# Kernel optimization log

Hardware: AMD Instinct MI355X
Metric: run time of the kernel (lower is better)

## Reference

```python
import jax, jax.numpy as jnp
import numpy as np

GROUPS = 32
EPS = 1e-5


def setup_inputs() -> dict:
    key = jax.random.key(0)
    k1, k2, k3, k4, k5 = jax.random.split(key, 5)
    B, C, H, W = 16, 256, 80, 80
    cg = C // GROUPS  # 8 channels per group
    x = jax.random.normal(k1, (B, C, H, W), dtype=jnp.float32)
    # conv1x1: Conv2d(cg, cg, 1) -> weight [cg, cg], bias [cg]
    fan_in = cg
    bound = 1.0 / np.sqrt(fan_in)
    conv_w = jax.random.uniform(k2, (cg, cg), minval=-bound, maxval=bound, dtype=jnp.float32)
    conv_b = jax.random.uniform(k3, (cg,), minval=-bound, maxval=bound, dtype=jnp.float32)
    # GroupNorm(num_groups=cg, num_channels=cg) affine params (init: ones/zeros)
    gn_w = jnp.ones((cg,), dtype=jnp.float32)
    gn_b = jnp.zeros((cg,), dtype=jnp.float32)
    return {"x": x, "conv_w": conv_w, "conv_b": conv_b, "gn_w": gn_w, "gn_b": gn_b}


def reference(x, conv_w, conv_b, gn_w, gn_b):
    b, c, h, w = x.shape
    cg = c // GROUPS
    gx = x.reshape(b * GROUPS, cg, h, w)  # [bg, cg, h, w]

    def norm(t):
        # GroupNorm with num_groups == num_channels: per-channel norm over (h, w)
        mu = jnp.mean(t, axis=(2, 3), keepdims=True)
        var = jnp.var(t, axis=(2, 3), keepdims=True)
        tn = (t - mu) * jax.lax.rsqrt(var + EPS)
        return tn * gn_w[None, :, None, None] + gn_b[None, :, None, None]

    def gate_branch(ph, pw):
        # ph: [bg, cg, h] (pooled over w), pw: [bg, cg, w] (pooled over h)
        cat = jnp.concatenate([ph, pw], axis=2)  # [bg, cg, h+w]
        hw = jnp.einsum('bcl,oc->bol', cat, conv_w) + conv_b[None, :, None]
        gh, gw = hw[:, :, :h], hw[:, :, h:]
        gated = gx * jax.nn.sigmoid(gh)[..., None] * jax.nn.sigmoid(gw)[:, :, None, :]
        return norm(gated)

    # avg-pool branch
    x1 = gate_branch(jnp.mean(gx, axis=3), jnp.mean(gx, axis=2))
    # max-pool branch
    y1 = gate_branch(jnp.max(gx, axis=3), jnp.max(gx, axis=2))

    x11 = x1.reshape(b * GROUPS, cg, h * w)
    y11 = y1.reshape(b * GROUPS, cg, h * w)
    # channel-attention vectors: softmax over the cg channel axis
    x12 = jax.nn.softmax(jnp.mean(x1, axis=(2, 3)), axis=-1)  # [bg, cg]  (avg pool)
    y12 = jax.nn.softmax(jnp.max(y1, axis=(2, 3)), axis=-1)   # [bg, cg]  (max pool)

    weights = jnp.einsum('bc,bcl->bl', x12, y11) + jnp.einsum('bc,bcl->bl', y12, x11)
    weights = weights.reshape(b * GROUPS, 1, h, w)
    return (gx * jax.nn.sigmoid(weights)).reshape(b, c, h, w)
```

## Files before the change

kernel.cpp:

```cpp
#include <hip/hip_runtime.h>
#include <math.h>

constexpr int CG   = 8;
constexpr int Hh   = 80;
constexpr int HW   = 6400;
constexpr int NG   = 512;
constexpr int NCH  = NG * CG;
constexpr int PP   = NCH * 80;
constexpr float EPSf = 1e-5f;

constexpr int COEF = 4 * PP;

__device__ __forceinline__ float sigmoidf(float v) {
    return 1.0f / (1.0f + __expf(-v));
}

__global__ __launch_bounds__(256) void k_pool(const float* __restrict__ x,
                                              float* __restrict__ ws) {
    const int bgc = blockIdx.x;
    const float* base = x + (size_t)bgc * HW;
    __shared__ float tile[Hh * 84];

    for (int v = threadIdx.x; v < 1600; v += 256) {
        int h  = v / 20;
        int w0 = (v % 20) * 4;
        float4 d = ((const float4*)base)[v];
        *(float4*)&tile[h * 84 + w0] = d;
    }
    __syncthreads();

    const int t = threadIdx.x;
    if (t < 80) {
        float s = 0.f, m = -INFINITY;
        const float4* r = (const float4*)&tile[t * 84];
        #pragma unroll
        for (int i = 0; i < 20; i++) {
            float4 d = r[i];
            s += d.x + d.y + d.z + d.w;
            m = fmaxf(m, fmaxf(fmaxf(d.x, d.y), fmaxf(d.z, d.w)));
        }
        ws[0 * PP + bgc * 80 + t] = s * (1.f / 80.f);
        ws[2 * PP + bgc * 80 + t] = m;
    } else if (t >= 128 && t < 208) {
        const int c = t - 128;
        float s2 = 0.f, m2 = -INFINITY;
        #pragma unroll 8
        for (int i = 0; i < 80; i++) {
            float v = tile[i * 84 + c];
            s2 += v;
            m2 = fmaxf(m2, v);
        }
        ws[1 * PP + bgc * 80 + c] = s2 * (1.f / 80.f);
        ws[3 * PP + bgc * 80 + c] = m2;
    }
}

__global__ __launch_bounds__(512) void k_mid(const float* __restrict__ x,
                                             const float* __restrict__ conv_w,
                                             const float* __restrict__ conv_b,
                                             const float* __restrict__ gnw,
                                             const float* __restrict__ gnb,
                                             float* __restrict__ ws) {
    const int bg  = blockIdx.x;
    const int tid = threadIdx.x;

    __shared__ float pl[4 * 640];
    __shared__ float g[4 * 640];
    __shared__ float wsm[64];
    __shared__ float cbs[8];
    __shared__ float stats[8][6];
    __shared__ float Axs[8], Bxs[8], Ays[8], Bys[8], ymaxs[8], cHx[8], cHy[8];
    __shared__ float kcs;

    if (tid < 64) wsm[tid] = conv_w[tid];
    if (tid < 8)  cbs[tid] = conv_b[tid];

    #pragma unroll
    for (int i = 0; i < 5; ++i) {
        const int e = tid + i * 512;
        if (e < 2560) {
            const int a = e / 640, rem = e % 640, c = rem / 80, p = rem % 80;
            pl[e] = ws[a * PP + (bg * 8 + c) * 80 + p];
        }
    }
    __syncthreads();

    #pragma unroll
    for (int i = 0; i < 5; ++i) {
        const int e = tid + i * 512;
        if (e < 2560) {
            const int rem = e % 640, a = e / 640, c = rem / 80, p = rem % 80;
            float acc = cbs[c];
            #pragma unroll
            for (int cc = 0; cc < 8; ++cc)
                acc += wsm[c * 8 + cc] * pl[a * 640 + cc * 80 + p];
            g[e] = sigmoidf(acc);
        }
    }
    __syncthreads();

    {
        const int c = tid >> 6, lane = tid & 63;
        const float* cb_ = x + (size_t)(bg * 8 + c) * HW;
        float s1x = 0.f, s2x = 0.f, s1y = 0.f, s2y = 0.f;
        float my = -INFINITY, ny = INFINITY;
        for (int j = 0; j < 25; ++j) {
            const int v = lane + j * 64;
            float4 d = ((const float4*)cb_)[v];
            const int h = v / 20, w0 = (v % 20) * 4;
            const float ghx = g[0 * 640 + c * 80 + h];
            const float ghy = g[2 * 640 + c * 80 + h];
            const float4 gwx = *(const float4*)&g[1 * 640 + c * 80 + w0];
            const float4 gwy = *(const float4*)&g[3 * 640 + c * 80 + w0];
            const float dd[4]  = {d.x, d.y, d.z, d.w};
            const float gx4[4] = {gwx.x, gwx.y, gwx.z, gwx.w};
            const float gy4[4] = {gwy.x, gwy.y, gwy.z, gwy.w};
            #pragma unroll
            for (int k = 0; k < 4; ++k) {
                const float tx = dd[k] * ghx * gx4[k];
                const float ty = dd[k] * ghy * gy4[k];
                s1x += tx; s2x += tx * tx;
                s1y += ty; s2y += ty * ty;
                my = fmaxf(my, ty); ny = fminf(ny, ty);
            }
        }
        #pragma unroll
        for (int off = 32; off > 0; off >>= 1) {
            s1x += __shfl_down(s1x, off);
            s2x += __shfl_down(s2x, off);
            s1y += __shfl_down(s1y, off);
            s2y += __shfl_down(s2y, off);
            my = fmaxf(my, __shfl_down(my, off));
            ny = fminf(ny, __shfl_down(ny, off));
        }
        if (lane == 0) {
            stats[c][0] = s1x; stats[c][1] = s2x; stats[c][2] = s1y;
            stats[c][3] = s2y; stats[c][4] = my;  stats[c][5] = ny;
        }
    }
    __syncthreads();

    if (tid < 8) {
        const float s1x = stats[tid][0], s2x = stats[tid][1];
        const float s1y = stats[tid][2], s2y = stats[tid][3];
        const float my  = stats[tid][4], ny  = stats[tid][5];
        const float w = gnw[tid], b = gnb[tid];
        const float mux  = s1x * (1.f / 6400.f);
        const float varx = s2x * (1.f / 6400.f) - mux * mux;
        const float ax   = rsqrtf(varx + EPSf) * w;
        Axs[tid] = ax; Bxs[tid] = b - mux * ax;
        const float muy  = s1y * (1.f / 6400.f);
        const float vary = s2y * (1.f / 6400.f) - muy * muy;
        const float ay   = rsqrtf(vary + EPSf) * w;
        Ays[tid] = ay; Bys[tid] = b - muy * ay;
        ymaxs[tid] = (ay >= 0.f ? my : ny) * ay + Bys[tid];
    }
    __syncthreads();
    if (tid == 0) {
        float x12[8], y12[8];
        float mb = -INFINITY;
        for (int c = 0; c < 8; ++c) mb = fmaxf(mb, gnb[c]);
        float se = 0.f;
        for (int c = 0; c < 8; ++c) { x12[c] = __expf(gnb[c] - mb); se += x12[c]; }
        float inv = 1.f / se;
        for (int c = 0; c < 8; ++c) x12[c] *= inv;
        float m2 = -INFINITY;
        for (int c = 0; c < 8; ++c) m2 = fmaxf(m2, ymaxs[c]);
        se = 0.f;
        for (int c = 0; c < 8; ++c) { y12[c] = __expf(ymaxs[c] - m2); se += y12[c]; }
        inv = 1.f / se;
        float kc = 0.f;
        for (int c = 0; c < 8; ++c) {
            y12[c] *= inv;
            cHx[c] = y12[c] * Axs[c];
            cHy[c] = x12[c] * Ays[c];
            kc += x12[c] * Bys[c] + y12[c] * Bxs[c];
        }
        kcs = kc;
    }
    __syncthreads();
    for (int e = tid; e < 640; e += 512) {
        g[e]        *= cHx[e / 80];
        g[1280 + e] *= cHy[e / 80];
    }
    __syncthreads();

    float* cf = ws + COEF + (size_t)bg * 2568;
    #pragma unroll
    for (int i = 0; i < 5; ++i) {
        const int e = tid + i * 512;
        if (e < 2560) cf[e] = g[e];
    }
    if (tid == 0) cf[2560] = kcs;
}

__global__ __launch_bounds__(256) void k_out(const float* __restrict__ x,
                                             const float* __restrict__ ws,
                                             float* __restrict__ out) {
    const int bg = blockIdx.x >> 2;
    const int q  = blockIdx.x & 3;
    const int tid = threadIdx.x;

    __shared__ float g[2560];
    __shared__ float kcs;
    const float* cf = ws + COEF + (size_t)bg * 2568;
    #pragma unroll
    for (int i = 0; i < 10; ++i) {
        const int e = tid + i * 256;
        if (e < 2560) g[e] = cf[e];
    }
    if (tid == 0) kcs = cf[2560];
    __syncthreads();

    const float kc = kcs;
    const float* base = x + (size_t)bg * CG * HW;
    float*       ob   = out + (size_t)bg * CG * HW;

    #pragma unroll
    for (int i = 0; i < 2; ++i) {
        const int v = q * 400 + tid + i * 256;
        if (v < (q + 1) * 400) {
            const int h = v / 20, w0 = (v % 20) * 4;
            float4 gxv[8];
            #pragma unroll
            for (int c = 0; c < 8; ++c)
                gxv[c] = *(const float4*)(base + c * HW + v * 4);

            float s0 = kc, s1 = kc, s2 = kc, s3 = kc;
            #pragma unroll
            for (int c = 0; c < 8; ++c) {
                const float chx = g[0 * 640 + c * 80 + h];
                const float chy = g[2 * 640 + c * 80 + h];
                const float4 cwx = *(const float4*)&g[1 * 640 + c * 80 + w0];
                const float4 cwy = *(const float4*)&g[3 * 640 + c * 80 + w0];
                s0 += gxv[c].x * (chy * cwy.x + chx * cwx.x);
                s1 += gxv[c].y * (chy * cwy.y + chx * cwx.y);
                s2 += gxv[c].z * (chy * cwy.z + chx * cwx.z);
                s3 += gxv[c].w * (chy * cwy.w + chx * cwx.w);
            }
            s0 = sigmoidf(s0); s1 = sigmoidf(s1);
            s2 = sigmoidf(s2); s3 = sigmoidf(s3);
            #pragma unroll
            for (int c = 0; c < 8; ++c) {
                float4 o;
                o.x = gxv[c].x * s0; o.y = gxv[c].y * s1;
                o.z = gxv[c].z * s2; o.w = gxv[c].w * s3;
                *(float4*)(ob + c * HW + v * 4) = o;
            }
        }
    }
}

extern "C" void kernel_launch(void* const* d_in, const int* in_sizes, int n_in,
                              void* d_out, int out_size, void* d_ws, size_t ws_size,
                              hipStream_t stream) {
    const float* x      = (const float*)d_in[0];
    const float* conv_w = (const float*)d_in[1];
    const float* conv_b = (const float*)d_in[2];
    const float* gn_w   = (const float*)d_in[3];
    const float* gn_b   = (const float*)d_in[4];
    float* out = (float*)d_out;
    float* ws  = (float*)d_ws;

    k_pool<<<NCH,    256, 0, stream>>>(x, ws);
    k_mid <<<NG,     512, 0, stream>>>(x, conv_w, conv_b, gn_w, gn_b, ws);
    k_out <<<NG * 4, 256, 0, stream>>>(x, ws, out);
}
```

Measured before the change: 79.27 us.

## Fuse mid and output kernels, keeping the group's x tile in registers

Merges k_mid and k_out into a single 1024-thread kernel per group. Each thread loads its slice of x (8 channels by up to 2 float4 positions) into registers once and reuses it for the gated-statistics pass and the final output pass. This removes a second full read of x and the round trip of the coefficients through the workspace. In exchange it uses only 512 blocks with heavy register pressure (64 floats of x per thread plus 1024-thread blocks), and the statistics reduction now goes across 16 waves per channel.

```diff
diff --git a/kernel.cpp b/kernel.cpp
--- a/kernel.cpp
+++ b/kernel.cpp
@@ -8,8 +8,6 @@
 constexpr int NCH  = NG * CG;
 constexpr int PP   = NCH * 80;
 constexpr float EPSf = 1e-5f;
-
-constexpr int COEF = 4 * PP;
 
 __device__ __forceinline__ float sigmoidf(float v) {
     return 1.0f / (1.0f + __expf(-v));
@@ -55,41 +53,53 @@
     }
 }
 
-__global__ __launch_bounds__(512) void k_mid(const float* __restrict__ x,
-                                             const float* __restrict__ conv_w,
-                                             const float* __restrict__ conv_b,
-                                             const float* __restrict__ gnw,
-                                             const float* __restrict__ gnb,
-                                             float* __restrict__ ws) {
+__global__ __launch_bounds__(1024, 4) void k_rest(
+    const float* __restrict__ x,
+    const float* __restrict__ conv_w,
+    const float* __restrict__ conv_b,
+    const float* __restrict__ gnw,
+    const float* __restrict__ gnb,
+    const float* __restrict__ ws,
+    float* __restrict__ out)
+{
     const int bg  = blockIdx.x;
     const int tid = threadIdx.x;
 
-    __shared__ float pl[4 * 640];
-    __shared__ float g[4 * 640];
+    __shared__ float pl[2560];
+    __shared__ float g[2560];
     __shared__ float wsm[64];
     __shared__ float cbs[8];
-    __shared__ float stats[8][6];
+    __shared__ float red[16][8][6];
     __shared__ float Axs[8], Bxs[8], Ays[8], Bys[8], ymaxs[8], cHx[8], cHy[8];
     __shared__ float kcs;
 
     if (tid < 64) wsm[tid] = conv_w[tid];
     if (tid < 8)  cbs[tid] = conv_b[tid];
-
-    #pragma unroll
-    for (int i = 0; i < 5; ++i) {
-        const int e = tid + i * 512;
+    #pragma unroll
+    for (int i = 0; i < 3; ++i) {
+        const int e = tid + i * 1024;
         if (e < 2560) {
             const int a = e / 640, rem = e % 640, c = rem / 80, p = rem % 80;
             pl[e] = ws[a * PP + (bg * 8 + c) * 80 + p];
         }
     }
-    __syncthreads();
-
-    #pragma unroll
-    for (int i = 0; i < 5; ++i) {
-        const int e = tid + i * 512;
+
+    const float* base = x + (size_t)bg * CG * HW;
+    const int s0 = tid, s1 = tid + 1024;
+    float4 xr0[8], xr1[8];
+    #pragma unroll
+    for (int c = 0; c < 8; ++c) xr0[c] = ((const float4*)(base + c * HW))[s0];
+    if (tid < 576) {
+        #pragma unroll
+        for (int c = 0; c < 8; ++c) xr1[c] = ((const float4*)(base + c * HW))[s1];
+    }
+    __syncthreads();
+
+    #pragma unroll
+    for (int i = 0; i < 3; ++i) {
+        const int e = tid + i * 1024;
         if (e < 2560) {
-            const int rem = e % 640, a = e / 640, c = rem / 80, p = rem % 80;
+            const int a = e / 640, rem = e % 640, c = rem / 80, p = rem % 80;
             float acc = cbs[c];
             #pragma unroll
             for (int cc = 0; cc < 8; ++cc)
@@ -99,20 +109,18 @@
     }
     __syncthreads();
 
-    {
-        const int c = tid >> 6, lane = tid & 63;
-        const float* cb_ = x + (size_t)(bg * 8 + c) * HW;
+    const int h0 = s0 / 20, w00 = (s0 % 20) * 4;
+    const int h1 = s1 / 20, w01 = (s1 % 20) * 4;
+    const int wv = tid >> 6, lane = tid & 63;
+    #pragma unroll
+    for (int c = 0; c < 8; ++c) {
         float s1x = 0.f, s2x = 0.f, s1y = 0.f, s2y = 0.f;
         float my = -INFINITY, ny = INFINITY;
-        for (int j = 0; j < 25; ++j) {
-            const int v = lane + j * 64;
-            float4 d = ((const float4*)cb_)[v];
-            const int h = v / 20, w0 = (v % 20) * 4;
-            const float ghx = g[0 * 640 + c * 80 + h];
-            const float ghy = g[2 * 640 + c * 80 + h];
-            const float4 gwx = *(const float4*)&g[1 * 640 + c * 80 + w0];
-            const float4 gwy = *(const float4*)&g[3 * 640 + c * 80 + w0];
-            const float dd[4]  = {d.x, d.y, d.z, d.w};
+        {
+            const float ghx = g[c * 80 + h0],  ghy = g[1280 + c * 80 + h0];
+            const float4 gwx = *(const float4*)&g[640  + c * 80 + w00];
+            const float4 gwy = *(const float4*)&g[1920 + c * 80 + w00];
+            const float dd[4]  = {xr0[c].x, xr0[c].y, xr0[c].z, xr0[c].w};
             const float gx4[4] = {gwx.x, gwx.y, gwx.z, gwx.w};
             const float gy4[4] = {gwy.x, gwy.y, gwy.z, gwy.w};
             #pragma unroll
@@ -124,6 +132,22 @@
                 my = fmaxf(my, ty); ny = fminf(ny, ty);
             }
         }
+        if (tid < 576) {
+            const float ghx = g[c * 80 + h1],  ghy = g[1280 + c * 80 + h1];
+            const float4 gwx = *(const float4*)&g[640  + c * 80 + w01];
+            const float4 gwy = *(const float4*)&g[1920 + c * 80 + w01];
+            const float dd[4]  = {xr1[c].x, xr1[c].y, xr1[c].z, xr1[c].w};
+            const float gx4[4] = {gwx.x, gwx.y, gwx.z, gwx.w};
+            const float gy4[4] = {gwy.x, gwy.y, gwy.z, gwy.w};
+            #pragma unroll
+            for (int k = 0; k < 4; ++k) {
+                const float tx = dd[k] * ghx * gx4[k];
+                const float ty = dd[k] * ghy * gy4[k];
+                s1x += tx; s2x += tx * tx;
+                s1y += ty; s2y += ty * ty;
+                my = fmaxf(my, ty); ny = fminf(ny, ty);
+            }
+        }
         #pragma unroll
         for (int off = 32; off > 0; off >>= 1) {
             s1x += __shfl_down(s1x, off);
@@ -134,26 +158,32 @@
             ny = fminf(ny, __shfl_down(ny, off));
         }
         if (lane == 0) {
-            stats[c][0] = s1x; stats[c][1] = s2x; stats[c][2] = s1y;
-            stats[c][3] = s2y; stats[c][4] = my;  stats[c][5] = ny;
+            red[wv][c][0] = s1x; red[wv][c][1] = s2x; red[wv][c][2] = s1y;
+            red[wv][c][3] = s2y; red[wv][c][4] = my;  red[wv][c][5] = ny;
         }
     }
     __syncthreads();
 
     if (tid < 8) {
-        const float s1x = stats[tid][0], s2x = stats[tid][1];
-        const float s1y = stats[tid][2], s2y = stats[tid][3];
-        const float my  = stats[tid][4], ny  = stats[tid][5];
+        float a0 = 0.f, a1 = 0.f, a2 = 0.f, a3 = 0.f;
+        float a4 = -INFINITY, a5 = INFINITY;
+        #pragma unroll
+        for (int w2 = 0; w2 < 16; ++w2) {
+            a0 += red[w2][tid][0]; a1 += red[w2][tid][1];
+            a2 += red[w2][tid][2]; a3 += red[w2][tid][3];
+            a4 = fmaxf(a4, red[w2][tid][4]);
+            a5 = fminf(a5, red[w2][tid][5]);
+        }
         const float w = gnw[tid], b = gnb[tid];
-        const float mux  = s1x * (1.f / 6400.f);
-        const float varx = s2x * (1.f / 6400.f) - mux * mux;
+        const float mux  = a0 * (1.f / 6400.f);
+        const float varx = a1 * (1.f / 6400.f) - mux * mux;
         const float ax   = rsqrtf(varx + EPSf) * w;
         Axs[tid] = ax; Bxs[tid] = b - mux * ax;
-        const float muy  = s1y * (1.f / 6400.f);
-        const float vary = s2y * (1.f / 6400.f) - muy * muy;
+        const float muy  = a2 * (1.f / 6400.f);
+        const float vary = a3 * (1.f / 6400.f) - muy * muy;
         const float ay   = rsqrtf(vary + EPSf) * w;
         Ays[tid] = ay; Bys[tid] = b - muy * ay;
-        ymaxs[tid] = (ay >= 0.f ? my : ny) * ay + Bys[tid];
+        ymaxs[tid] = (ay >= 0.f ? a4 : a5) * ay + Bys[tid];
     }
     __syncthreads();
     if (tid == 0) {
@@ -179,74 +209,56 @@
         kcs = kc;
     }
     __syncthreads();
-    for (int e = tid; e < 640; e += 512) {
-        g[e]        *= cHx[e / 80];
-        g[1280 + e] *= cHy[e / 80];
-    }
-    __syncthreads();
-
-    float* cf = ws + COEF + (size_t)bg * 2568;
-    #pragma unroll
-    for (int i = 0; i < 5; ++i) {
-        const int e = tid + i * 512;
-        if (e < 2560) cf[e] = g[e];
-    }
-    if (tid == 0) cf[2560] = kcs;
-}
-
-__global__ __launch_bounds__(256) void k_out(const float* __restrict__ x,
-                                             const float* __restrict__ ws,
-                                             float* __restrict__ out) {
-    const int bg = blockIdx.x >> 2;
-    const int q  = blockIdx.x & 3;
-    const int tid = threadIdx.x;
-
-    __shared__ float g[2560];
-    __shared__ float kcs;
-    const float* cf = ws + COEF + (size_t)bg * 2568;
-    #pragma unroll
-    for (int i = 0; i < 10; ++i) {
-        const int e = tid + i * 256;
-        if (e < 2560) g[e] = cf[e];
-    }
-    if (tid == 0) kcs = cf[2560];
+    if (tid < 640) {
+        g[tid]        *= cHx[tid / 80];
+        g[1280 + tid] *= cHy[tid / 80];
+    }
     __syncthreads();
 
     const float kc = kcs;
-    const float* base = x + (size_t)bg * CG * HW;
-    float*       ob   = out + (size_t)bg * CG * HW;
-
-    #pragma unroll
-    for (int i = 0; i < 2; ++i) {
-        const int v = q * 400 + tid + i * 256;
-        if (v < (q + 1) * 400) {
-            const int h = v / 20, w0 = (v % 20) * 4;
-            float4 gxv[8];
-            #pragma unroll
-            for (int c = 0; c < 8; ++c)
-                gxv[c] = *(const float4*)(base + c * HW + v * 4);
-
-            float s0 = kc, s1 = kc, s2 = kc, s3 = kc;
-            #pragma unroll
-            for (int c = 0; c < 8; ++c) {
-                const float chx = g[0 * 640 + c * 80 + h];
-                const float chy = g[2 * 640 + c * 80 + h];
-                const float4 cwx = *(const float4*)&g[1 * 640 + c * 80 + w0];
-                const float4 cwy = *(const float4*)&g[3 * 640 + c * 80 + w0];
-                s0 += gxv[c].x * (chy * cwy.x + chx * cwx.x);
-                s1 += gxv[c].y * (chy * cwy.y + chx * cwx.y);
-                s2 += gxv[c].z * (chy * cwy.z + chx * cwx.z);
-                s3 += gxv[c].w * (chy * cwy.w + chx * cwx.w);
-            }
-            s0 = sigmoidf(s0); s1 = sigmoidf(s1);
-            s2 = sigmoidf(s2); s3 = sigmoidf(s3);
-            #pragma unroll
-            for (int c = 0; c < 8; ++c) {
-                float4 o;
-                o.x = gxv[c].x * s0; o.y = gxv[c].y * s1;
-                o.z = gxv[c].z * s2; o.w = gxv[c].w * s3;
-                *(float4*)(ob + c * HW + v * 4) = o;
-            }
+    float* ob = out + (size_t)bg * CG * HW;
+    {
+        float u0 = kc, u1 = kc, u2 = kc, u3 = kc;
+        #pragma unroll
+        for (int c = 0; c < 8; ++c) {
+            const float chx = g[c * 80 + h0], chy = g[1280 + c * 80 + h0];
+            const float4 cwx = *(const float4*)&g[640  + c * 80 + w00];
+            const float4 cwy = *(const float4*)&g[1920 + c * 80 + w00];
+            u0 += xr0[c].x * (chy * cwy.x + chx * cwx.x);
+            u1 += xr0[c].y * (chy * cwy.y + chx * cwx.y);
+            u2 += xr0[c].z * (chy * cwy.z + chx * cwx.z);
+            u3 += xr0[c].w * (chy * cwy.w + chx * cwx.w);
+        }
+        u0 = sigmoidf(u0); u1 = sigmoidf(u1);
+        u2 = sigmoidf(u2); u3 = sigmoidf(u3);
+        #pragma unroll
+        for (int c = 0; c < 8; ++c) {
+            float4 o;
+            o.x = xr0[c].x * u0; o.y = xr0[c].y * u1;
+            o.z = xr0[c].z * u2; o.w = xr0[c].w * u3;
+            ((float4*)(ob + c * HW))[s0] = o;
+        }
+    }
+    if (tid < 576) {
+        float u0 = kc, u1 = kc, u2 = kc, u3 = kc;
+        #pragma unroll
+        for (int c = 0; c < 8; ++c) {
+            const float chx = g[c * 80 + h1], chy = g[1280 + c * 80 + h1];
+            const float4 cwx = *(const float4*)&g[640  + c * 80 + w01];
+            const float4 cwy = *(const float4*)&g[1920 + c * 80 + w01];
+            u0 += xr1[c].x * (chy * cwy.x + chx * cwx.x);
+            u1 += xr1[c].y * (chy * cwy.y + chx * cwx.y);
+            u2 += xr1[c].z * (chy * cwy.z + chx * cwx.z);
+            u3 += xr1[c].w * (chy * cwy.w + chx * cwx.w);
+        }
+        u0 = sigmoidf(u0); u1 = sigmoidf(u1);
+        u2 = sigmoidf(u2); u3 = sigmoidf(u3);
+        #pragma unroll
+        for (int c = 0; c < 8; ++c) {
+            float4 o;
+            o.x = xr1[c].x * u0; o.y = xr1[c].y * u1;
+            o.z = xr1[c].z * u2; o.w = xr1[c].w * u3;
+            ((float4*)(ob + c * HW))[s1] = o;
         }
     }
 }
@@ -262,7 +274,6 @@
     float* out = (float*)d_out;
     float* ws  = (float*)d_ws;
 
-    k_pool<<<NCH,    256, 0, stream>>>(x, ws);
-    k_mid <<<NG,     512, 0, stream>>>(x, conv_w, conv_b, gn_w, gn_b, ws);
-    k_out <<<NG * 4, 256, 0, stream>>>(x, ws, out);
-}
+    k_pool<<<NCH, 256, 0, stream>>>(x, ws);
+    k_rest<<<NG, 1024, 0, stream>>>(x, conv_w, conv_b, gn_w, gn_b, ws, out);
+}
```

Result: slower. 96.77 us (+22.1%).

## Fuse mid and output kernels into a single 1024-thread per-group kernel

Applied to the files above, without the earlier changes.

Merges the statistics/coefficient kernel and the output kernel into one kernel with 1024-thread blocks per group, so the coefficients stay in shared memory instead of going through a global workspace round trip and a third launch. The group's x slab (8 channels, about 200KB) is read twice within the same block, which may hit in L2. The trade-off is fewer blocks (512 instead of 2048 for the output phase), so there is less parallelism and the output phase has to wait behind the per-block reduction.

```diff
diff --git a/kernel.cpp b/kernel.cpp
--- a/kernel.cpp
+++ b/kernel.cpp
@@ -8,8 +8,6 @@
 constexpr int NCH  = NG * CG;
 constexpr int PP   = NCH * 80;
 constexpr float EPSf = 1e-5f;
-
-constexpr int COEF = 4 * PP;
 
 __device__ __forceinline__ float sigmoidf(float v) {
     return 1.0f / (1.0f + __expf(-v));
@@ -55,29 +53,31 @@
     }
 }
 
-__global__ __launch_bounds__(512) void k_mid(const float* __restrict__ x,
-                                             const float* __restrict__ conv_w,
-                                             const float* __restrict__ conv_b,
-                                             const float* __restrict__ gnw,
-                                             const float* __restrict__ gnb,
-                                             float* __restrict__ ws) {
+__global__ __launch_bounds__(1024, 4) void k_rest(
+    const float* __restrict__ x,
+    const float* __restrict__ conv_w,
+    const float* __restrict__ conv_b,
+    const float* __restrict__ gnw,
+    const float* __restrict__ gnb,
+    const float* __restrict__ ws,
+    float* __restrict__ out)
+{
     const int bg  = blockIdx.x;
     const int tid = threadIdx.x;
 
-    __shared__ float pl[4 * 640];
-    __shared__ float g[4 * 640];
+    __shared__ float pl[2560];
+    __shared__ float g[2560];
     __shared__ float wsm[64];
     __shared__ float cbs[8];
-    __shared__ float stats[8][6];
+    __shared__ float red[16][6];
     __shared__ float Axs[8], Bxs[8], Ays[8], Bys[8], ymaxs[8], cHx[8], cHy[8];
     __shared__ float kcs;
 
     if (tid < 64) wsm[tid] = conv_w[tid];
     if (tid < 8)  cbs[tid] = conv_b[tid];
-
     #pragma unroll
-    for (int i = 0; i < 5; ++i) {
-        const int e = tid + i * 512;
+    for (int i = 0; i < 3; ++i) {
+        const int e = tid + i * 1024;
         if (e < 2560) {
             const int a = e / 640, rem = e % 640, c = rem / 80, p = rem % 80;
             pl[e] = ws[a * PP + (bg * 8 + c) * 80 + p];
@@ -86,10 +86,10 @@
     __syncthreads();
 
     #pragma unroll
-    for (int i = 0; i < 5; ++i) {
-        const int e = tid + i * 512;
+    for (int i = 0; i < 3; ++i) {
+        const int e = tid + i * 1024;
         if (e < 2560) {
-            const int rem = e % 640, a = e / 640, c = rem / 80, p = rem % 80;
+            const int a = e / 640, rem = e % 640, c = rem / 80, p = rem % 80;
             float acc = cbs[c];
             #pragma unroll
             for (int cc = 0; cc < 8; ++cc)
@@ -99,29 +99,33 @@
     }
     __syncthreads();
 
+    const float* base = x + (size_t)bg * CG * HW;
     {
-        const int c = tid >> 6, lane = tid & 63;
-        const float* cb_ = x + (size_t)(bg * 8 + c) * HW;
+        const int c = tid >> 7, sl = tid & 127;
+        const float* cb_ = base + c * HW;
         float s1x = 0.f, s2x = 0.f, s1y = 0.f, s2y = 0.f;
         float my = -INFINITY, ny = INFINITY;
-        for (int j = 0; j < 25; ++j) {
-            const int v = lane + j * 64;
-            float4 d = ((const float4*)cb_)[v];
-            const int h = v / 20, w0 = (v % 20) * 4;
-            const float ghx = g[0 * 640 + c * 80 + h];
-            const float ghy = g[2 * 640 + c * 80 + h];
-            const float4 gwx = *(const float4*)&g[1 * 640 + c * 80 + w0];
-            const float4 gwy = *(const float4*)&g[3 * 640 + c * 80 + w0];
-            const float dd[4]  = {d.x, d.y, d.z, d.w};
-            const float gx4[4] = {gwx.x, gwx.y, gwx.z, gwx.w};
-            const float gy4[4] = {gwy.x, gwy.y, gwy.z, gwy.w};
-            #pragma unroll
-            for (int k = 0; k < 4; ++k) {
-                const float tx = dd[k] * ghx * gx4[k];
-                const float ty = dd[k] * ghy * gy4[k];
-                s1x += tx; s2x += tx * tx;
-                s1y += ty; s2y += ty * ty;
-                my = fmaxf(my, ty); ny = fminf(ny, ty);
+        #pragma unroll 4
+        for (int j = 0; j < 13; ++j) {
+            const int v = sl + j * 128;
+            if (v < 1600) {
+                float4 d = ((const float4*)cb_)[v];
+                const int h = v / 20, w0 = (v % 20) * 4;
+                const float ghx = g[0 * 640 + c * 80 + h];
+                const float ghy = g[2 * 640 + c * 80 + h];
+                const float4 gwx = *(const float4*)&g[1 * 640 + c * 80 + w0];
+                const float4 gwy = *(const float4*)&g[3 * 640 + c * 80 + w0];
+                const float dd[4]  = {d.x, d.y, d.z, d.w};
+                const float gx4[4] = {gwx.x, gwx.y, gwx.z, gwx.w};
+                const float gy4[4] = {gwy.x, gwy.y, gwy.z, gwy.w};
+                #pragma unroll
+                for (int k = 0; k < 4; ++k) {
+                    const float tx = dd[k] * ghx * gx4[k];
+                    const float ty = dd[k] * ghy * gy4[k];
+                    s1x += tx; s2x += tx * tx;
+                    s1y += ty; s2y += ty * ty;
+                    my = fmaxf(my, ty); ny = fminf(ny, ty);
+                }
             }
         }
         #pragma unroll
@@ -133,17 +137,21 @@
             my = fmaxf(my, __shfl_down(my, off));
             ny = fminf(ny, __shfl_down(ny, off));
         }
-        if (lane == 0) {
-            stats[c][0] = s1x; stats[c][1] = s2x; stats[c][2] = s1y;
-            stats[c][3] = s2y; stats[c][4] = my;  stats[c][5] = ny;
+        const int wv = tid >> 6;
+        if ((tid & 63) == 0) {
+            red[wv][0] = s1x; red[wv][1] = s2x; red[wv][2] = s1y;
+            red[wv][3] = s2y; red[wv][4] = my;  red[wv][5] = ny;
         }
     }
     __syncthreads();
 
     if (tid < 8) {
-        const float s1x = stats[tid][0], s2x = stats[tid][1];
-        const float s1y = stats[tid][2], s2y = stats[tid][3];
-        const float my  = stats[tid][4], ny  = stats[tid][5];
+        const float s1x = red[2 * tid][0] + red[2 * tid + 1][0];
+        const float s2x = red[2 * tid][1] + red[2 * tid + 1][1];
+        const float s1y = red[2 * tid][2] + red[2 * tid + 1][2];
+        const float s2y = red[2 * tid][3] + red[2 * tid + 1][3];
+        const float my  = fmaxf(red[2 * tid][4], red[2 * tid + 1][4]);
+        const float ny  = fminf(red[2 * tid][5], red[2 * tid + 1][5]);
         const float w = gnw[tid], b = gnb[tid];
         const float mux  = s1x * (1.f / 6400.f);
         const float varx = s2x * (1.f / 6400.f) - mux * mux;
@@ -179,60 +187,31 @@
         kcs = kc;
     }
     __syncthreads();
-    for (int e = tid; e < 640; e += 512) {
-        g[e]        *= cHx[e / 80];
-        g[1280 + e] *= cHy[e / 80];
-    }
-    __syncthreads();
-
-    float* cf = ws + COEF + (size_t)bg * 2568;
-    #pragma unroll
-    for (int i = 0; i < 5; ++i) {
-        const int e = tid + i * 512;
-        if (e < 2560) cf[e] = g[e];
-    }
-    if (tid == 0) cf[2560] = kcs;
-}
-
-__global__ __launch_bounds__(256) void k_out(const float* __restrict__ x,
-                                             const float* __restrict__ ws,
-                                             float* __restrict__ out) {
-    const int bg = blockIdx.x >> 2;
-    const int q  = blockIdx.x & 3;
-    const int tid = threadIdx.x;
-
-    __shared__ float g[2560];
-    __shared__ float kcs;
-    const float* cf = ws + COEF + (size_t)bg * 2568;
-    #pragma unroll
-    for (int i = 0; i < 10; ++i) {
-        const int e = tid + i * 256;
-        if (e < 2560) g[e] = cf[e];
-    }
-    if (tid == 0) kcs = cf[2560];
+    if (tid < 640) {
+        g[tid]        *= cHx[tid / 80];
+        g[1280 + tid] *= cHy[tid / 80];
+    }
     __syncthreads();
 
     const float kc = kcs;
-    const float* base = x + (size_t)bg * CG * HW;
-    float*       ob   = out + (size_t)bg * CG * HW;
-
+    float* ob = out + (size_t)bg * CG * HW;
     #pragma unroll
     for (int i = 0; i < 2; ++i) {
-        const int v = q * 400 + tid + i * 256;
-        if (v < (q + 1) * 400) {
+        const int v = tid + i * 1024;
+        if (v < 1600) {
             const int h = v / 20, w0 = (v % 20) * 4;
             float4 gxv[8];
             #pragma unroll
             for (int c = 0; c < 8; ++c)
-                gxv[c] = *(const float4*)(base + c * HW + v * 4);
+                gxv[c] = ((const float4*)(base + c * HW))[v];
 
             float s0 = kc, s1 = kc, s2 = kc, s3 = kc;
             #pragma unroll
             for (int c = 0; c < 8; ++c) {
-                const float chx = g[0 * 640 + c * 80 + h];
-                const float chy = g[2 * 640 + c * 80 + h];
-                const float4 cwx = *(const float4*)&g[1 * 640 + c * 80 + w0];
-                const float4 cwy = *(const float4*)&g[3 * 640 + c * 80 + w0];
+                const float chx = g[c * 80 + h];
+                const float chy = g[1280 + c * 80 + h];
+                const float4 cwx = *(const float4*)&g[640  + c * 80 + w0];
+                const float4 cwy = *(const float4*)&g[1920 + c * 80 + w0];
                 s0 += gxv[c].x * (chy * cwy.x + chx * cwx.x);
                 s1 += gxv[c].y * (chy * cwy.y + chx * cwx.y);
                 s2 += gxv[c].z * (chy * cwy.z + chx * cwx.z);
@@ -245,7 +224,7 @@
                 float4 o;
                 o.x = gxv[c].x * s0; o.y = gxv[c].y * s1;
                 o.z = gxv[c].z * s2; o.w = gxv[c].w * s3;
-                *(float4*)(ob + c * HW + v * 4) = o;
+                ((float4*)(ob + c * HW))[v] = o;
             }
         }
     }
@@ -262,7 +241,6 @@
     float* out = (float*)d_out;
     float* ws  = (float*)d_ws;
 
-    k_pool<<<NCH,    256, 0, stream>>>(x, ws);
-    k_mid <<<NG,     512, 0, stream>>>(x, conv_w, conv_b, gn_w, gn_b, ws);
-    k_out <<<NG * 4, 256, 0, stream>>>(x, ws, out);
-}
+    k_pool<<<NCH, 256, 0, stream>>>(x, ws);
+    k_rest<<<NG, 1024, 0, stream>>>(x, conv_w, conv_b, gn_w, gn_b, ws, out);
+}
```

New measurement: 72.58 us. 1.09x faster.
